# Performance work log

Measured on AMD Instinct MI355X. Metric: run time of the kernel, lower is better.

## Reference

```python
import jax, jax.numpy as jnp
import numpy as np


def _node_layer(X, Z, adj_v, T, W, b, p):
    # d_e = (Z @ p^T): per-edge scalar; multiplier = T diag(d_e) T^T  (Nv,Nv)
    d = (Z @ p.T)[:, 0]
    mult = (T * d[None, :]) @ T.T
    n = mult.shape[0]
    idx = jnp.arange(n)
    M = mult.at[idx, idx].set(1.0)           # diagonal forced to 1
    A = M * adj_v
    A = A / jnp.max(A, axis=0, keepdims=True)  # column-max normalization
    return A @ (X @ W) + b, Z


def _edge_layer(X, Z, adj_e, T, W, b, p):
    # d_v = (X @ p^T): per-node scalar; multiplier = T^T diag(d_v) T  (Ne,Ne)
    d = (X @ p.T)[:, 0]
    mult = (T.T * d[None, :]) @ T
    n = mult.shape[0]
    idx = jnp.arange(n)
    M = mult.at[idx, idx].set(1.0)
    A = M * adj_e
    A = A / jnp.max(A, axis=0, keepdims=True)
    return X, A @ (Z @ W) + b


def setup_inputs() -> dict:
    key = jax.random.key(0)
    ks = jax.random.split(key, 16)
    B, Nv, Ne = 16, 1024, 2048
    Fv, Fe, H, C = 128, 64, 128, 16
    inp = {
        "X": jax.random.normal(ks[0], (B, Nv, Fv), jnp.float32),
        "Z": jax.random.normal(ks[1], (B, Ne, Fe), jnp.float32),
        "adj_e": jax.random.uniform(ks[2], (B, Ne, Ne), jnp.float32, 0.01, 1.0),
        "adj_v": jax.random.uniform(ks[3], (B, Nv, Nv), jnp.float32, 0.01, 1.0),
        "T": jax.random.uniform(ks[4], (B, Nv, Ne), jnp.float32),
        # gc1: node layer  nfeat_v -> nhid, p over edge features
        "W1": jax.random.normal(ks[5], (Fv, H), jnp.float32) * 0.05,
        "b1": jnp.zeros((H,), jnp.float32),
        "p1": jax.random.normal(ks[6], (1, Fe), jnp.float32),
        # gc2: edge layer  nfeat_e -> nfeat_e, p over node features (nhid)
        "W2": jax.random.normal(ks[7], (Fe, Fe), jnp.float32) * 0.05,
        "b2": jnp.zeros((Fe,), jnp.float32),
        "p2": jax.random.normal(ks[8], (1, H), jnp.float32),
        # gc3: node layer  nhid -> nclass
        "W3": jax.random.normal(ks[9], (H, C), jnp.float32) * 0.05,
        "b3": jnp.zeros((C,), jnp.float32),
        "p3": jax.random.normal(ks[10], (1, Fe), jnp.float32),
    }
    return inp


def reference(X, Z, adj_e, adj_v, T, W1, b1, p1, W2, b2, p2, W3, b3, p3):
    # dropout is identity in eval mode
    def single(x, z, ae, av, t):
        x1, z1 = _node_layer(x, z, av, t, W1, b1, p1)
        x1, z1 = jax.nn.relu(x1), jax.nn.relu(z1)
        x2, z2 = _edge_layer(x1, z1, ae, t, W2, b2, p2)
        x2, z2 = jax.nn.relu(x2), jax.nn.relu(z2)
        x3, _ = _node_layer(x2, z2, av, t, W3, b3, p3)
        return x3
    return jax.vmap(single)(X, Z, adj_e, adj_v, T)  # (B, Nv, nclass)
```

## Files before the change

### kernel.cpp

```cpp
#include <hip/hip_runtime.h>
#include <hip/hip_bf16.h>
#include <stdint.h>

#define DEVI __device__ __forceinline__

typedef __bf16 bf16x8_t __attribute__((ext_vector_type(8)));
typedef float f32x4_t __attribute__((ext_vector_type(4)));
typedef unsigned short u16;

static constexpr int NBATCH = 16;
static constexpr int NV = 1024;
static constexpr int NE = 2048;
static constexpr int FV = 128;
static constexpr int FE = 64;
static constexpr int HID = 128;
static constexpr int NCLS = 16;

DEVI u16 f2bf(float f) { __hip_bfloat16 h = __float2bfloat16(f); return *reinterpret_cast<u16*>(&h); }
DEVI float bf2f(u16 u) { union { unsigned int i; float f; } x; x.i = ((unsigned int)u) << 16; return x.f; }

DEVI void gload_lds16(const void* g, void* l) {
  __builtin_amdgcn_global_load_lds(
      (const __attribute__((address_space(1))) unsigned int*)g,
      (__attribute__((address_space(3))) unsigned int*)l, 16, 0, 0);
}

template <bool WRITE_ASC>
__global__ void k_transpose(const float* __restrict__ T, u16* __restrict__ Tbf,
                            u16* __restrict__ Ttbf, const float* __restrict__ d1,
                            u16* __restrict__ Asc1) {
  __shared__ u16 s[32][33];
  const int b = blockIdx.z;
  const int e0 = blockIdx.x * 32, v0 = blockIdx.y * 32;
  const float* Tb = T + (size_t)b * NV * NE;
  u16* T1 = Tbf + (size_t)b * NV * NE;
  u16* T2 = Ttbf + (size_t)b * NE * NV;
  const int tx = threadIdx.x & 31, ty = threadIdx.x >> 5;
  float dv = 0.f;
  if (WRITE_ASC) dv = d1[(size_t)b * NE + e0 + tx];
  #pragma unroll
  for (int i = 0; i < 4; ++i) {
    int v = v0 + ty + i * 8;
    float f = Tb[(size_t)v * NE + e0 + tx];
    u16 u = f2bf(f);
    T1[(size_t)v * NE + e0 + tx] = u;
    if (WRITE_ASC) Asc1[(size_t)b * NV * NE + (size_t)v * NE + e0 + tx] = f2bf(f * dv);
    s[ty + i * 8][tx] = u;
  }
  __syncthreads();
  #pragma unroll
  for (int i = 0; i < 4; ++i) {
    int e = e0 + ty + i * 8;
    T2[(size_t)e * NV + v0 + tx] = s[tx][ty + i * 8];
  }
}

__global__ void k_rowdot(const float* __restrict__ In, const float* __restrict__ p,
                         float* __restrict__ d, int R, int C) {
  const int b = blockIdx.y;
  const int w = threadIdx.x >> 6, l = threadIdx.x & 63;
  const int r = blockIdx.x * 4 + w;
  const float* row = In + ((size_t)b * R + r) * C;
  float s = 0.f;
  for (int c = l; c < C; c += 64) s += row[c] * p[c];
  #pragma unroll
  for (int o = 32; o; o >>= 1) s += __shfl_xor(s, o);
  if (l == 0) d[(size_t)b * R + r] = s;
}

__global__ void k_scale(const u16* __restrict__ In, const float* __restrict__ d,
                        u16* __restrict__ Out, int K, int b0) {
  const int bi = blockIdx.y, bg = b0 + bi;
  const size_t elems = (size_t)NV * NE;
  const size_t idx = ((size_t)blockIdx.x * 256 + threadIdx.x) * 8;
  const float* dd = d + (size_t)bg * K;
  const int k = (int)(idx & (size_t)(K - 1));
  const u16* in = In + (size_t)bg * elems + idx;
  uint4 raw = *(const uint4*)in;
  float f[8];
  f[0] = bf2f(raw.x & 0xffff); f[1] = bf2f(raw.x >> 16);
  f[2] = bf2f(raw.y & 0xffff); f[3] = bf2f(raw.y >> 16);
  f[4] = bf2f(raw.z & 0xffff); f[5] = bf2f(raw.z >> 16);
  f[6] = bf2f(raw.w & 0xffff); f[7] = bf2f(raw.w >> 16);
  u16 o[8];
  #pragma unroll
  for (int t = 0; t < 8; ++t) o[t] = f2bf(f[t] * dd[k + t]);
  *(uint4*)((u16*)Out + (size_t)bi * elems + idx) = *(uint4*)o;
}

__global__ __launch_bounds__(512, 2) void k_gemm256(
    const u16* __restrict__ A, size_t sA, int ldA,
    const u16* __restrict__ Bm, size_t sB, int ldB,
    int M, int K,
    const float* __restrict__ adj, u16* __restrict__ Pout,
    float* __restrict__ pmax, int b0) {
  extern __shared__ __align__(16) char smem[];
  const int gx = gridDim.x, gy = gridDim.y;
  const int total = gx * gy * gridDim.z;
  int orig = blockIdx.x + gx * (blockIdx.y + gy * blockIdx.z);
  const int cpx = total >> 3;
  int swz = (orig & 7) * cpx + (orig >> 3);
  const int bx = swz % gx;
  const int by = (swz / gx) % gy;
  const int bi = swz / (gx * gy);
  const int bg = b0 + bi;

  const u16* Ab = A + (size_t)bi * sA;
  const u16* Bb = Bm + (size_t)bg * sB;
  const int tm = by * 256, tn = bx * 256;
  const int tid = threadIdx.x, wid = tid >> 6, l = tid & 63;
  const int wr = wid >> 2, wc = wid & 3;

  const int srow = tid >> 3;
  const int scol = (((tid & 7) ^ (srow & 7)) << 3);

  const int Lx = (l & 7) << 4;
  const int colb0 = (((l >> 4) << 4)) ^ Lx;
  const int colb1 = (64 + ((l >> 4) << 4)) ^ Lx;
  const int arowb = (wr * 128 + (l & 15)) * 128;
  const int browb = (wc * 64 + (l & 15)) * 128;

  auto stage = [&](int buf, int k0) {
    char* ab = smem + (buf << 16);
    char* bb = ab + 32768;
    #pragma unroll
    for (int ld2 = 0; ld2 < 4; ++ld2) {
      gload_lds16(Ab + (size_t)(tm + ld2 * 64 + srow) * ldA + (k0 + scol),
                  ab + ld2 * 8192 + tid * 16);
      gload_lds16(Bb + (size_t)(tn + ld2 * 64 + srow) * ldB + (k0 + scol),
                  bb + ld2 * 8192 + tid * 16);
    }
  };

  f32x4_t acc[8][4];
  const f32x4_t zv = {0.f, 0.f, 0.f, 0.f};
  #pragma unroll
  for (int m = 0; m < 8; ++m)
    #pragma unroll
    for (int n = 0; n < 4; ++n) acc[m][n] = zv;

  const int NT = K >> 6;
  stage(0, 0);
  __syncthreads();

  for (int kt = 0; kt < NT; ++kt) {
    const int buf = kt & 1;
    if (kt + 1 < NT) stage(buf ^ 1, (kt + 1) << 6);
    char* abase = smem + (buf << 16);
    char* bbase = abase + 32768;
    bf16x8_t af[4][2], bfr[4][2];
    #pragma unroll
    for (int m = 0; m < 4; ++m) {
      af[m][0] = *(const bf16x8_t*)(abase + arowb + m * 2048 + colb0);
      af[m][1] = *(const bf16x8_t*)(abase + arowb + m * 2048 + colb1);
    }
    #pragma unroll
    for (int n = 0; n < 2; ++n) {
      bfr[n][0] = *(const bf16x8_t*)(bbase + browb + n * 2048 + colb0);
      bfr[n][1] = *(const bf16x8_t*)(bbase + browb + n * 2048 + colb1);
    }
    __builtin_amdgcn_s_setprio(1);
    #pragma unroll
    for (int m = 0; m < 4; ++m)
      #pragma unroll
      for (int n = 0; n < 2; ++n)
        #pragma unroll
        for (int kk = 0; kk < 2; ++kk)
          acc[m][n] = __builtin_amdgcn_mfma_f32_16x16x32_bf16(af[m][kk], bfr[n][kk], acc[m][n], 0, 0, 0);
    __builtin_amdgcn_s_setprio(0);
    #pragma unroll
    for (int n = 2; n < 4; ++n) {
      bfr[n][0] = *(const bf16x8_t*)(bbase + browb + n * 2048 + colb0);
      bfr[n][1] = *(const bf16x8_t*)(bbase + browb + n * 2048 + colb1);
    }
    __builtin_amdgcn_s_setprio(1);
    #pragma unroll
    for (int m = 0; m < 4; ++m)
      #pragma unroll
      for (int n = 2; n < 4; ++n)
        #pragma unroll
        for (int kk = 0; kk < 2; ++kk)
          acc[m][n] = __builtin_amdgcn_mfma_f32_16x16x32_bf16(af[m][kk], bfr[n][kk], acc[m][n], 0, 0, 0);
    __builtin_amdgcn_s_setprio(0);
    #pragma unroll
    for (int m = 0; m < 4; ++m) {
      af[m][0] = *(const bf16x8_t*)(abase + arowb + (m + 4) * 2048 + colb0);
      af[m][1] = *(const bf16x8_t*)(abase + arowb + (m + 4) * 2048 + colb1);
    }
    __builtin_amdgcn_s_setprio(1);
    #pragma unroll
    for (int m = 0; m < 4; ++m)
      #pragma unroll
      for (int n = 2; n < 4; ++n)
        #pragma unroll
        for (int kk = 0; kk < 2; ++kk)
          acc[m + 4][n] = __builtin_amdgcn_mfma_f32_16x16x32_bf16(af[m][kk], bfr[n][kk], acc[m + 4][n], 0, 0, 0);
    __builtin_amdgcn_s_setprio(0);
    __builtin_amdgcn_s_setprio(1);
    #pragma unroll
    for (int m = 0; m < 4; ++m)
      #pragma unroll
      for (int n = 0; n < 2; ++n)
        #pragma unroll
        for (int kk = 0; kk < 2; ++kk)
          acc[m + 4][n] = __builtin_amdgcn_mfma_f32_16x16x32_bf16(af[m][kk], bfr[n][kk], acc[m + 4][n], 0, 0, 0);
    __builtin_amdgcn_s_setprio(0);
    __syncthreads();
  }

  const float* adjb = adj + (size_t)bg * M * M;
  u16* Pb = Pout + (size_t)bi * (size_t)M * M;
  float vmax[4] = {0.f, 0.f, 0.f, 0.f};
  #pragma unroll
  for (int m = 0; m < 8; ++m)
    #pragma unroll
    for (int n = 0; n < 4; ++n)
      #pragma unroll
      for (int q = 0; q < 4; ++q) {
        int row = tm + wr * 128 + m * 16 + (l >> 4) * 4 + q;
        int col = tn + wc * 64 + n * 16 + (l & 15);
        float v = acc[m][n][q];
        if (row == col) v = 1.0f;
        v *= adjb[(size_t)row * M + col];
        vmax[n] = fmaxf(vmax[n], v);
        Pb[(size_t)row * M + col] = f2bf(v);
      }
  #pragma unroll
  for (int n = 0; n < 4; ++n) {
    vmax[n] = fmaxf(vmax[n], __shfl_xor(vmax[n], 16));
    vmax[n] = fmaxf(vmax[n], __shfl_xor(vmax[n], 32));
  }
  float* red = (float*)smem;
  if (l < 16) {
    #pragma unroll
    for (int n = 0; n < 4; ++n)
      red[((wr * 4 + wc) * 4 + n) * 16 + l] = vmax[n];
  }
  __syncthreads();
  if (wr == 0 && l < 16) {
    #pragma unroll
    for (int n = 0; n < 4; ++n) {
      float a = red[((0 * 4 + wc) * 4 + n) * 16 + l];
      float b = red[((1 * 4 + wc) * 4 + n) * 16 + l];
      pmax[((size_t)bi * gy + by) * M + tn + wc * 64 + n * 16 + l] = fmaxf(a, b);
    }
  }
}

__global__ void k_colmax2(const float* __restrict__ pmax, float* __restrict__ c,
                          int N, int G, int b0) {
  const int bi = blockIdx.y, bg = b0 + bi;
  const int j = blockIdx.x * 256 + threadIdx.x;
  const float* pb = pmax + (size_t)bi * G * N;
  float m = 0.f;
  for (int g = 0; g < G; ++g) m = fmaxf(m, pb[(size_t)g * N + j]);
  c[(size_t)bg * N + j] = m;
}

template <int EPI>
__global__ __launch_bounds__(256) void k_gemm(
    const u16* __restrict__ A, size_t sA, int ldA,
    const u16* __restrict__ Bm, size_t sB, int ldB,
    int M, int K, int Nrows, int Ncols,
    const float* __restrict__ bias, float* __restrict__ Fout, int b0) {
  __shared__ __align__(16) u16 As[2][128 * 32];
  __shared__ __align__(16) u16 Bs[2][128 * 32];
  const int bi = blockIdx.z, bg = b0 + bi;
  const u16* Ab = A + (size_t)bi * sA;
  const u16* Bb = Bm + (size_t)bg * sB;
  const int tm = blockIdx.y * 128, tn = blockIdx.x * 128;
  const int tid = threadIdx.x, w = tid >> 6, l = tid & 63;
  const int wm = (w >> 1) * 64, wn = (w & 1) * 64;
  const int lr = l & 15, kg = (l >> 4) * 8;
  const int chunk = l & 3;
  int arow[2], brow[2];
  #pragma unroll
  for (int i = 0; i < 2; ++i) {
    int r = (i * 4 + w) * 16 + (l >> 2);
    arow[i] = tm + r;
    int rb = tn + r;
    brow[i] = rb < Nrows ? rb : Nrows - 1;
  }
  f32x4_t acc[4][4];
  const f32x4_t zv = {0.f, 0.f, 0.f, 0.f};
  #pragma unroll
  for (int m = 0; m < 4; ++m)
    #pragma unroll
    for (int n = 0; n < 4; ++n) acc[m][n] = zv;

  auto stage = [&](int buf, int k0) {
    #pragma unroll
    for (int i = 0; i < 2; ++i) {
      gload_lds16(Ab + (size_t)arow[i] * ldA + k0 + chunk * 8,
                  (char*)As[buf] + (i * 4 + w) * 1024);
      gload_lds16(Bb + (size_t)brow[i] * ldB + k0 + chunk * 8,
                  (char*)Bs[buf] + (i * 4 + w) * 1024);
    }
  };

  const int nsteps = K >> 5;
  stage(0, 0);
  __syncthreads();
  for (int s = 0; s < nsteps; ++s) {
    const int cur = s & 1;
    if (s + 1 < nsteps) stage(cur ^ 1, (s + 1) << 5);
    bf16x8_t af[4], bfr[4];
    #pragma unroll
    for (int m = 0; m < 4; ++m) af[m] = *(const bf16x8_t*)&As[cur][(wm + m * 16 + lr) * 32 + kg];
    #pragma unroll
    for (int n = 0; n < 4; ++n) bfr[n] = *(const bf16x8_t*)&Bs[cur][(wn + n * 16 + lr) * 32 + kg];
    #pragma unroll
    for (int m = 0; m < 4; ++m)
      #pragma unroll
      for (int n = 0; n < 4; ++n)
        acc[m][n] = __builtin_amdgcn_mfma_f32_16x16x32_bf16(af[m], bfr[n], acc[m][n], 0, 0, 0);
    __syncthreads();
  }

  float* Ob = Fout + (size_t)bg * M * Ncols;
  #pragma unroll
  for (int m = 0; m < 4; ++m)
    #pragma unroll
    for (int n = 0; n < 4; ++n)
      #pragma unroll
      for (int q = 0; q < 4; ++q) {
        int row = tm + wm + m * 16 + (l >> 4) * 4 + q;
        int col = tn + wn + n * 16 + lr;
        if (col < Ncols) {
          float v = acc[m][n][q] + bias[col];
          if (EPI == 1) v = fmaxf(v, 0.f);
          Ob[(size_t)row * Ncols + col] = v;
        }
      }
}

template <int EPI>
__global__ __launch_bounds__(256) void k_gemmPY(
    const u16* __restrict__ A, size_t sA, int ldA,
    const u16* __restrict__ Bm, size_t sB,
    int M, int K, int Ncols,
    const float* __restrict__ bias, float* __restrict__ Fout, int b0) {
  __shared__ __align__(16) u16 As[2][128 * 32];
  __shared__ __align__(16) u16 Bs[2][64 * 32];
  const int bi = blockIdx.z, bg = b0 + bi;
  const u16* Ab = A + (size_t)bi * sA;
  const u16* Bb = Bm + (size_t)bg * sB;
  const int tm = blockIdx.y * 128;
  const int tid = threadIdx.x, w = tid >> 6, l = tid & 63;
  const int wm = (w >> 1) * 64, wn = (w & 1) * 32;
  const int lr = l & 15, kg = (l >> 4) * 8;
  const int chunk = l & 3;
  int arow[2];
  #pragma unroll
  for (int i = 0; i < 2; ++i) arow[i] = tm + (i * 4 + w) * 16 + (l >> 2);
  const int brow = w * 16 + (l >> 2);

  f32x4_t acc[4][2];
  const f32x4_t zv = {0.f, 0.f, 0.f, 0.f};
  #pragma unroll
  for (int m = 0; m < 4; ++m)
    #pragma unroll
    for (int n = 0; n < 2; ++n) acc[m][n] = zv;

  auto stage = [&](int buf, int k0) {
    #pragma unroll
    for (int i = 0; i < 2; ++i)
      gload_lds16(Ab + (size_t)arow[i] * ldA + k0 + chunk * 8,
                  (char*)As[buf] + (i * 4 + w) * 1024);
    gload_lds16(Bb + (size_t)brow * ldA  + k0 + chunk * 8,
                (char*)Bs[buf] + tid * 16);
  };

  const int nsteps = K >> 5;
  stage(0, 0);
  __syncthreads();
  for (int s = 0; s < nsteps; ++s) {
    const int cur = s & 1;
    if (s + 1 < nsteps) stage(cur ^ 1, (s + 1) << 5);
    bf16x8_t af[4], bfr[2];
    #pragma unroll
    for (int m = 0; m < 4; ++m) af[m] = *(const bf16x8_t*)&As[cur][(wm + m * 16 + lr) * 32 + kg];
    #pragma unroll
    for (int n = 0; n < 2; ++n) bfr[n] = *(const bf16x8_t*)&Bs[cur][(wn + n * 16 + lr) * 32 + kg];
    #pragma unroll
    for (int m = 0; m < 4; ++m)
      #pragma unroll
      for (int n = 0; n < 2; ++n)
        acc[m][n] = __builtin_amdgcn_mfma_f32_16x16x32_bf16(af[m], bfr[n], acc[m][n], 0, 0, 0);
    __syncthreads();
  }

  float* Ob = Fout + (size_t)bg * M * Ncols;
  #pragma unroll
  for (int m = 0; m < 4; ++m)
    #pragma unroll
    for (int n = 0; n < 2; ++n)
      #pragma unroll
      for (int q = 0; q < 4; ++q) {
        int row = tm + wm + m * 16 + (l >> 4) * 4 + q;
        int col = wn + n * 16 + lr;
        if (col < Ncols) {
          float v = acc[m][n][q] + bias[col];
          if (EPI == 1) v = fmaxf(v, 0.f);
          Ob[(size_t)row * Ncols + col] = v;
        }
      }
}

template <bool RELU_IN>
__global__ __launch_bounds__(256) void k_smallgemm(
    const float* __restrict__ X, size_t sX, int Kd,
    const float* __restrict__ W, int Cc,
    const float* __restrict__ cmax, u16* __restrict__ YT, size_t sY,
    int Nj, int b0) {
  __shared__ float Xs[64][129];
  __shared__ float Ws[128][33];
  const int bg = b0 + blockIdx.y;
  const float* Xb = X + (size_t)bg * sX;
  const int j0 = blockIdx.x * 64;
  const int tid = threadIdx.x;
  for (int idx = tid; idx < 64 * (Kd / 4); idx += 256) {
    int r = idx / (Kd / 4), q = idx % (Kd / 4);
    float4 v = *(const float4*)(Xb + (size_t)(j0 + r) * Kd + q * 4);
    if (RELU_IN) {
      v.x = fmaxf(v.x, 0.f); v.y = fmaxf(v.y, 0.f);
      v.z = fmaxf(v.z, 0.f); v.w = fmaxf(v.w, 0.f);
    }
    Xs[r][q * 4 + 0] = v.x; Xs[r][q * 4 + 1] = v.y;
    Xs[r][q * 4 + 2] = v.z; Xs[r][q * 4 + 3] = v.w;
  }
  const int r = tid & 63, cg = tid >> 6;
  const float rinv = 1.0f / cmax[(size_t)bg * Nj + j0 + r];
  for (int c0 = 0; c0 < Cc; c0 += 32) {
    __syncthreads();
    for (int idx = tid; idx < Kd * 32; idx += 256) {
      int k = idx >> 5, c = c0 + (idx & 31);
      Ws[k][idx & 31] = (c < Cc) ? W[(size_t)k * Cc + c] : 0.f;
    }
    __syncthreads();
    float acc[8] = {0.f, 0.f, 0.f, 0.f, 0.f, 0.f, 0.f, 0.f};
    for (int k = 0; k < Kd; ++k) {
      float xv = Xs[r][k];
      #pragma unroll
      for (int cc = 0; cc < 8; ++cc) acc[cc] += xv * Ws[k][cg * 8 + cc];
    }
    #pragma unroll
    for (int cc = 0; cc < 8; ++cc) {
      int c = c0 + cg * 8 + cc;
      if (c < Cc) YT[(size_t)bg * sY + (size_t)c * Nj + j0 + r] = f2bf(acc[cc] * rinv);
    }
  }
}

extern "C" void kernel_launch(void* const* d_in, const int* in_sizes, int n_in,
                              void* d_out, int out_size, void* d_ws, size_t ws_size,
                              hipStream_t stream) {
  const float* X    = (const float*)d_in[0];
  const float* Z    = (const float*)d_in[1];
  const float* adje = (const float*)d_in[2];
  const float* adjv = (const float*)d_in[3];
  const float* T    = (const float*)d_in[4];
  const float* W1   = (const float*)d_in[5];
  const float* b1   = (const float*)d_in[6];
  const float* p1   = (const float*)d_in[7];
  const float* W2   = (const float*)d_in[8];
  const float* b2   = (const float*)d_in[9];
  const float* p2   = (const float*)d_in[10];
  const float* W3   = (const float*)d_in[11];
  const float* b3   = (const float*)d_in[12];
  const float* p3   = (const float*)d_in[13];
  float* out = (float*)d_out;
  (void)in_sizes; (void)n_in; (void)out_size;

  hipFuncSetAttribute(reinterpret_cast<const void*>(k_gemm256),
                      hipFuncAttributeMaxDynamicSharedMemorySize, 131072);

  char* ws = (char*)d_ws;
  size_t off = 0;
  auto alloc = [&](size_t n) -> char* {
    char* p = ws + off; off = (off + n + 255) & ~(size_t)255; return p;
  };
  u16* Tbf    = (u16*)alloc((size_t)NBATCH * NV * NE * 2);
  u16* Ttbf   = (u16*)alloc((size_t)NBATCH * NE * NV * 2);
  float* dbuf = (float*)alloc((size_t)NBATCH * NE * 4);
  float* cbuf = (float*)alloc((size_t)NBATCH * NE * 4);
  float* pmax = (float*)alloc((size_t)NBATCH * 8 * NE * 4);
  u16* YT     = (u16*)alloc((size_t)NBATCH * NE * 64 * 2);
  float* x1   = (float*)alloc((size_t)NBATCH * NV * HID * 4);
  float* z2   = (float*)alloc((size_t)NBATCH * NE * FE * 4);
  const size_t needA = (size_t)NBATCH * NV * NE * 2;
  const size_t needP = (size_t)NBATCH * NE * NE * 2;
  const bool full = (ws_size >= off + needA + needP + 1024);
  const int nb = full ? NBATCH : 1;
  u16* Asc = (u16*)alloc(full ? needA : (size_t)NV * NE * 2);
  u16* P   = (u16*)alloc(full ? needP : (size_t)NE * NE * 2);

  const dim3 blk(256, 1, 1);
  const dim3 blk512(512, 1, 1);

  k_rowdot<<<dim3(NE / 4, NBATCH), blk, 0, stream>>>(Z, p1, dbuf, NE, FE);
  if (full)
    k_transpose<true><<<dim3(NE / 32, NV / 32, NBATCH), blk, 0, stream>>>(
        T, Tbf, Ttbf, dbuf, Asc);
  else
    k_transpose<false><<<dim3(NE / 32, NV / 32, NBATCH), blk, 0, stream>>>(
        T, Tbf, Ttbf, nullptr, nullptr);

  for (int b0 = 0; b0 < NBATCH; b0 += nb) {
    if (!full)
      k_scale<<<dim3((NV * NE) / 2048, nb), blk, 0, stream>>>(Tbf, dbuf, Asc, NE, b0);
    k_gemm256<<<dim3(NV / 256, NV / 256, nb), blk512, 131072, stream>>>(
        Asc, (size_t)NV * NE, NE, Tbf, (size_t)NV * NE, NE, NV, NE, adjv, P, pmax, b0);
    k_colmax2<<<dim3(NV / 256, nb), blk, 0, stream>>>(pmax, cbuf, NV, NV / 256, b0);
    k_smallgemm<false><<<dim3(NV / 64, nb), blk, 0, stream>>>(
        X, (size_t)NV * FV, FV, W1, HID, cbuf, YT, (size_t)NV * HID, NV, b0);
    k_gemm<1><<<dim3(1, NV / 128, nb), blk, 0, stream>>>(
        P, (size_t)NV * NV, NV, YT, (size_t)NV * HID, NV,
        NV, NV, HID, HID, b1, x1, b0);
  }
  k_rowdot<<<dim3(NV / 4, NBATCH), blk, 0, stream>>>(x1, p2, dbuf, NV, HID);
  for (int b0 = 0; b0 < NBATCH; b0 += nb) {
    k_scale<<<dim3((NE * NV) / 2048, nb), blk, 0, stream>>>(Ttbf, dbuf, Asc, NV, b0);
    k_gemm256<<<dim3(NE / 256, NE / 256, nb), blk512, 131072, stream>>>(
        Asc, (size_t)NE * NV, NV, Ttbf, (size_t)NE * NV, NV, NE, NV, adje, P, pmax, b0);
    k_colmax2<<<dim3(NE / 256, nb), blk, 0, stream>>>(pmax, cbuf, NE, NE / 256, b0);
    k_smallgemm<true><<<dim3(NE / 64, nb), blk, 0, stream>>>(
        Z, (size_t)NE * FE, FE, W2, FE, cbuf, YT, (size_t)NE * FE, NE, b0);
    k_gemmPY<1><<<dim3(1, NE / 128, nb), blk, 0, stream>>>(
        P, (size_t)NE * NE, NE, YT, (size_t)NE * FE,
        NE, NE, FE, b2, z2, b0);
  }
  k_rowdot<<<dim3(NE / 4, NBATCH), blk, 0, stream>>>(z2, p3, dbuf, NE, FE);
  for (int b0 = 0; b0 < NBATCH; b0 += nb) {
    k_scale<<<dim3((NV * NE) / 2048, nb), blk, 0, stream>>>(Tbf, dbuf, Asc, NE, b0);
    k_gemm256<<<dim3(NV / 256, NV / 256, nb), blk512, 131072, stream>>>(
        Asc, (size_t)NV * NE, NE, Tbf, (size_t)NV * NE, NE, NV, NE, adjv, P, pmax, b0);
    k_colmax2<<<dim3(NV / 256, nb), blk, 0, stream>>>(pmax, cbuf, NV, NV / 256, b0);
    k_smallgemm<false><<<dim3(NV / 64, nb), blk, 0, stream>>>(
        x1, (size_t)NV * HID, HID, W3, NCLS, cbuf, YT, (size_t)NV * NCLS, NV, b0);
    k_gemmPY<2><<<dim3(1, NV / 128, nb), blk, 0, stream>>>(
        P, (size_t)NV * NV, NV, YT, (size_t)NV * NCLS,
        NV, NV, NCLS, b3, out, b0);
  }
}
```

Baseline: 659.7 us.

## Use swizzled 128x128 GEMM for edge layer and fold column-max into smallgemm

Adds a 128x128-tile bf16 MFMA GEMM with an XCD-aware block swizzle and an LDS bank swizzle for the edge-layer multiplier product (K=1024). It replaces the 256x256 kernel on that stage to give more blocks and better occupancy. It also removes the separate k_colmax2 launch by having k_smallgemm reduce the per-tile partial column maxima itself. The pmax buffer doubles to hold 16 row-tile partials. The trade-off is more redundant A/B loads with smaller tiles, plus each smallgemm thread now reads G partials.

```diff
diff --git a/kernel.cpp b/kernel.cpp
--- a/kernel.cpp
+++ b/kernel.cpp
@@ -124,11 +124,11 @@
     char* ab = smem + (buf << 16);
     char* bb = ab + 32768;
     #pragma unroll
-    for (int ld2 = 0; ld2 < 4; ++ld2) {
-      gload_lds16(Ab + (size_t)(tm + ld2 * 64 + srow) * ldA + (k0 + scol),
-                  ab + ld2 * 8192 + tid * 16);
-      gload_lds16(Bb + (size_t)(tn + ld2 * 64 + srow) * ldB + (k0 + scol),
-                  bb + ld2 * 8192 + tid * 16);
+    for (int i = 0; i < 4; ++i) {
+      gload_lds16(Ab + (size_t)(tm + i * 64 + srow) * ldA + (k0 + scol),
+                  ab + i * 8192 + tid * 16);
+      gload_lds16(Bb + (size_t)(tn + i * 64 + srow) * ldB + (k0 + scol),
+                  bb + i * 8192 + tid * 16);
     }
   };
 
@@ -247,14 +247,117 @@
   }
 }
 
-__global__ void k_colmax2(const float* __restrict__ pmax, float* __restrict__ c,
-                          int N, int G, int b0) {
-  const int bi = blockIdx.y, bg = b0 + bi;
-  const int j = blockIdx.x * 256 + threadIdx.x;
-  const float* pb = pmax + (size_t)bi * G * N;
-  float m = 0.f;
-  for (int g = 0; g < G; ++g) m = fmaxf(m, pb[(size_t)g * N + j]);
-  c[(size_t)bg * N + j] = m;
+__global__ __launch_bounds__(256) void k_gemm128s(
+    const u16* __restrict__ A, size_t sA, int ldA,
+    const u16* __restrict__ Bm, size_t sB, int ldB,
+    int M, int K,
+    const float* __restrict__ adj, u16* __restrict__ Pout,
+    float* __restrict__ pmax, int b0) {
+  __shared__ __align__(16) u16 As[2][128 * 32];
+  __shared__ __align__(16) u16 Bs[2][128 * 32];
+  const int gx = gridDim.x, gy = gridDim.y;
+  const int total = gx * gy * gridDim.z;
+  int orig = blockIdx.x + gx * (blockIdx.y + gy * blockIdx.z);
+  const int cpx = total >> 3;
+  int swz = (orig & 7) * cpx + (orig >> 3);
+  const int bx = swz % gx;
+  const int by = (swz / gx) % gy;
+  const int bi = swz / (gx * gy);
+  const int bg = b0 + bi;
+
+  const u16* Ab = A + (size_t)bi * sA;
+  const u16* Bb = Bm + (size_t)bg * sB;
+  const int tm = by * 128, tn = bx * 128;
+  const int tid = threadIdx.x, wid = tid >> 6, l = tid & 63;
+  const int wm = (wid >> 1) * 64, wn = (wid & 1) * 64;
+  const int lr = l & 15;
+
+  const int srow = tid >> 2;
+  const int sc = tid & 3;
+  const int scol = ((sc ^ ((srow >> 1) & 3)) << 3);
+
+  const int slotx = (((l >> 4) ^ ((l >> 1) & 3)) << 4);
+  const int arowb = (wm + lr) * 64;
+  const int browb = (wn + lr) * 64;
+
+  auto stage = [&](int buf, int k0) {
+    #pragma unroll
+    for (int i = 0; i < 2; ++i) {
+      gload_lds16(Ab + (size_t)(tm + i * 64 + srow) * ldA + (k0 + scol),
+                  (char*)As[buf] + i * 4096 + tid * 16);
+      gload_lds16(Bb + (size_t)(tn + i * 64 + srow) * ldB + (k0 + scol),
+                  (char*)Bs[buf] + i * 4096 + tid * 16);
+    }
+  };
+
+  f32x4_t acc[4][4];
+  const f32x4_t zv = {0.f, 0.f, 0.f, 0.f};
+  #pragma unroll
+  for (int m = 0; m < 4; ++m)
+    #pragma unroll
+    for (int n = 0; n < 4; ++n) acc[m][n] = zv;
+
+  const int NT = K >> 5;
+  stage(0, 0);
+  __syncthreads();
+
+  for (int kt = 0; kt < NT; ++kt) {
+    const int buf = kt & 1;
+    if (kt + 1 < NT) stage(buf ^ 1, (kt + 1) << 5);
+    bf16x8_t af[4], bfr[4];
+    #pragma unroll
+    for (int m = 0; m < 4; ++m)
+      af[m] = *(const bf16x8_t*)((char*)As[buf] + arowb + m * 1024 + slotx);
+    #pragma unroll
+    for (int n = 0; n < 4; ++n)
+      bfr[n] = *(const bf16x8_t*)((char*)Bs[buf] + browb + n * 1024 + slotx);
+    __builtin_amdgcn_s_setprio(1);
+    #pragma unroll
+    for (int m = 0; m < 4; ++m)
+      #pragma unroll
+      for (int n = 0; n < 4; ++n)
+        acc[m][n] = __builtin_amdgcn_mfma_f32_16x16x32_bf16(af[m], bfr[n], acc[m][n], 0, 0, 0);
+    __builtin_amdgcn_s_setprio(0);
+    __syncthreads();
+  }
+
+  const float* adjb = adj + (size_t)bg * M * M;
+  u16* Pb = Pout + (size_t)bi * (size_t)M * M;
+  float vmax[4] = {0.f, 0.f, 0.f, 0.f};
+  #pragma unroll
+  for (int m = 0; m < 4; ++m)
+    #pragma unroll
+    for (int n = 0; n < 4; ++n)
+      #pragma unroll
+      for (int q = 0; q < 4; ++q) {
+        int row = tm + wm + m * 16 + (l >> 4) * 4 + q;
+        int col = tn + wn + n * 16 + lr;
+        float v = acc[m][n][q];
+        if (row == col) v = 1.0f;
+        v *= adjb[(size_t)row * M + col];
+        vmax[n] = fmaxf(vmax[n], v);
+        Pb[(size_t)row * M + col] = f2bf(v);
+      }
+  #pragma unroll
+  for (int n = 0; n < 4; ++n) {
+    vmax[n] = fmaxf(vmax[n], __shfl_xor(vmax[n], 16));
+    vmax[n] = fmaxf(vmax[n], __shfl_xor(vmax[n], 32));
+  }
+  float* red = (float*)As;
+  if (l < 16) {
+    #pragma unroll
+    for (int n = 0; n < 4; ++n)
+      red[(wid * 4 + n) * 16 + l] = vmax[n];
+  }
+  __syncthreads();
+  if ((wid >> 1) == 0 && l < 16) {
+    #pragma unroll
+    for (int n = 0; n < 4; ++n) {
+      float a = red[(wid * 4 + n) * 16 + l];
+      float b = red[((wid + 2) * 4 + n) * 16 + l];
+      pmax[((size_t)bi * gy + by) * M + tn + (wid & 1) * 64 + n * 16 + l] = fmaxf(a, b);
+    }
+  }
 }
 
 template <int EPI>
@@ -367,7 +470,7 @@
     for (int i = 0; i < 2; ++i)
       gload_lds16(Ab + (size_t)arow[i] * ldA + k0 + chunk * 8,
                   (char*)As[buf] + (i * 4 + w) * 1024);
-    gload_lds16(Bb + (size_t)brow * ldA  + k0 + chunk * 8,
+    gload_lds16(Bb + (size_t)brow * ldA + k0 + chunk * 8,
                 (char*)Bs[buf] + tid * 16);
   };
 
@@ -411,11 +514,11 @@
 __global__ __launch_bounds__(256) void k_smallgemm(
     const float* __restrict__ X, size_t sX, int Kd,
     const float* __restrict__ W, int Cc,
-    const float* __restrict__ cmax, u16* __restrict__ YT, size_t sY,
+    const float* __restrict__ pmax, int G, u16* __restrict__ YT, size_t sY,
     int Nj, int b0) {
   __shared__ float Xs[64][129];
   __shared__ float Ws[128][33];
-  const int bg = b0 + blockIdx.y;
+  const int bi = blockIdx.y, bg = b0 + bi;
   const float* Xb = X + (size_t)bg * sX;
   const int j0 = blockIdx.x * 64;
   const int tid = threadIdx.x;
@@ -430,7 +533,12 @@
     Xs[r][q * 4 + 2] = v.z; Xs[r][q * 4 + 3] = v.w;
   }
   const int r = tid & 63, cg = tid >> 6;
-  const float rinv = 1.0f / cmax[(size_t)bg * Nj + j0 + r];
+  float mx = 0.f;
+  {
+    const float* pb = pmax + (size_t)bi * G * Nj + (j0 + r);
+    for (int g = 0; g < G; ++g) mx = fmaxf(mx, pb[(size_t)g * Nj]);
+  }
+  const float rinv = 1.0f / mx;
   for (int c0 = 0; c0 < Cc; c0 += 32) {
     __syncthreads();
     for (int idx = tid; idx < Kd * 32; idx += 256) {
@@ -483,8 +591,7 @@
   u16* Tbf    = (u16*)alloc((size_t)NBATCH * NV * NE * 2);
   u16* Ttbf   = (u16*)alloc((size_t)NBATCH * NE * NV * 2);
   float* dbuf = (float*)alloc((size_t)NBATCH * NE * 4);
-  float* cbuf = (float*)alloc((size_t)NBATCH * NE * 4);
-  float* pmax = (float*)alloc((size_t)NBATCH * 8 * NE * 4);
+  float* pmax = (float*)alloc((size_t)NBATCH * 16 * NE * 4);
   u16* YT     = (u16*)alloc((size_t)NBATCH * NE * 64 * 2);
   float* x1   = (float*)alloc((size_t)NBATCH * NV * HID * 4);
   float* z2   = (float*)alloc((size_t)NBATCH * NE * FE * 4);
@@ -511,9 +618,8 @@
       k_scale<<<dim3((NV * NE) / 2048, nb), blk, 0, stream>>>(Tbf, dbuf, Asc, NE, b0);
     k_gemm256<<<dim3(NV / 256, NV / 256, nb), blk512, 131072, stream>>>(
         Asc, (size_t)NV * NE, NE, Tbf, (size_t)NV * NE, NE, NV, NE, adjv, P, pmax, b0);
-    k_colmax2<<<dim3(NV / 256, nb), blk, 0, stream>>>(pmax, cbuf, NV, NV / 256, b0);
     k_smallgemm<false><<<dim3(NV / 64, nb), blk, 0, stream>>>(
-        X, (size_t)NV * FV, FV, W1, HID, cbuf, YT, (size_t)NV * HID, NV, b0);
+        X, (size_t)NV * FV, FV, W1, HID, pmax, NV / 256, YT, (size_t)NV * HID, NV, b0);
     k_gemm<1><<<dim3(1, NV / 128, nb), blk, 0, stream>>>(
         P, (size_t)NV * NV, NV, YT, (size_t)NV * HID, NV,
         NV, NV, HID, HID, b1, x1, b0);
@@ -521,11 +627,10 @@
   k_rowdot<<<dim3(NV / 4, NBATCH), blk, 0, stream>>>(x1, p2, dbuf, NV, HID);
   for (int b0 = 0; b0 < NBATCH; b0 += nb) {
     k_scale<<<dim3((NE * NV) / 2048, nb), blk, 0, stream>>>(Ttbf, dbuf, Asc, NV, b0);
-    k_gemm256<<<dim3(NE / 256, NE / 256, nb), blk512, 131072, stream>>>(
+    k_gemm128s<<<dim3(NE / 128, NE / 128, nb), blk, 0, stream>>>(
         Asc, (size_t)NE * NV, NV, Ttbf, (size_t)NE * NV, NV, NE, NV, adje, P, pmax, b0);
-    k_colmax2<<<dim3(NE / 256, nb), blk, 0, stream>>>(pmax, cbuf, NE, NE / 256, b0);
     k_smallgemm<true><<<dim3(NE / 64, nb), blk, 0, stream>>>(
-        Z, (size_t)NE * FE, FE, W2, FE, cbuf, YT, (size_t)NE * FE, NE, b0);
+        Z, (size_t)NE * FE, FE, W2, FE, pmax, NE / 128, YT, (size_t)NE * FE, NE, b0);
     k_gemmPY<1><<<dim3(1, NE / 128, nb), blk, 0, stream>>>(
         P, (size_t)NE * NE, NE, YT, (size_t)NE * FE,
         NE, NE, FE, b2, z2, b0);
@@ -535,9 +640,8 @@
     k_scale<<<dim3((NV * NE) / 2048, nb), blk, 0, stream>>>(Tbf, dbuf, Asc, NE, b0);
     k_gemm256<<<dim3(NV / 256, NV / 256, nb), blk512, 131072, stream>>>(
         Asc, (size_t)NV * NE, NE, Tbf, (size_t)NV * NE, NE, NV, NE, adjv, P, pmax, b0);
-    k_colmax2<<<dim3(NV / 256, nb), blk, 0, stream>>>(pmax, cbuf, NV, NV / 256, b0);
     k_smallgemm<false><<<dim3(NV / 64, nb), blk, 0, stream>>>(
-        x1, (size_t)NV * HID, HID, W3, NCLS, cbuf, YT, (size_t)NV * NCLS, NV, b0);
+        x1, (size_t)NV * HID, HID, W3, NCLS, pmax, NV / 256, YT, (size_t)NV * NCLS, NV, b0);
     k_gemmPY<2><<<dim3(1, NV / 128, nb), blk, 0, stream>>>(
         P, (size_t)NV * NV, NV, YT, (size_t)NV * NCLS,
         NV, NV, NCLS, b3, out, b0);
```

After: 722.9 us. +9.6%, slower.
